# Performance work log

Measured on AMD Instinct MI355X. Metric: run time of the kernel, lower is better.

## Reference

```python
import jax, jax.numpy as jnp
import numpy as np

B, S, N, D, H = 4, 2048, 2048, 1024, 16
HD = D // H  # 64
EPS = 1e-5


def layer_norm(x, w, b):
    m = x.mean(axis=-1, keepdims=True)
    v = ((x - m) ** 2).mean(axis=-1, keepdims=True)
    return (x - m) / jnp.sqrt(v + EPS) * w + b


def setup_inputs() -> dict:
    key = jax.random.key(0)
    ks = jax.random.split(key, 4)
    x_q = jax.random.normal(ks[0], (B, S, D), dtype=jnp.float32)
    x_k = jax.random.normal(ks[1], (B, N, HD), dtype=jnp.float32)
    x_v = jax.random.normal(ks[2], (B, N, HD), dtype=jnp.float32)
    # learned params
    qn_w = jnp.ones((HD,), jnp.float32)
    qn_b = jnp.zeros((HD,), jnp.float32)
    kn_w = jnp.ones((HD,), jnp.float32)
    kn_b = jnp.zeros((HD,), jnp.float32)
    n_w = jnp.ones((D,), jnp.float32)
    n_b = jnp.zeros((D,), jnp.float32)
    # xavier-uniform proj weight (D, D), no bias (proj_bias=False)
    limit = np.sqrt(6.0 / (D + D))
    proj_w = jax.random.uniform(ks[3], (D, D), jnp.float32, -limit, limit)
    return {"x_q": x_q, "x_k": x_k, "x_v": x_v,
            "qn_w": qn_w, "qn_b": qn_b, "kn_w": kn_w, "kn_b": kn_b,
            "n_w": n_w, "n_b": n_b, "proj_w": proj_w}


def reference(x_q, x_k, x_v, qn_w, qn_b, kn_w, kn_b, n_w, n_b, proj_w):
    scale = HD ** -0.5
    # faithful to torch: q.reshape(B, H, -1, head_dim) -- NO transpose before reshape
    q = x_q.reshape(B, H, S, HD)
    q = layer_norm(q, qn_w, qn_b)
    k = layer_norm(x_k, kn_w, kn_b)
    q = q * scale
    attn = jnp.einsum('bhsd,bnd->bhsn', q, k)  # (B,H,S,N) shared K across heads
    attn = jax.nn.softmax(attn, axis=-1)
    x = jnp.einsum('bhsn,bnd->bhsd', attn, x_v)  # shared V across heads
    x = jnp.transpose(x, (0, 2, 1, 3)).reshape(B, S, D)
    x = layer_norm(x, n_w, n_b)
    x = x @ proj_w.T  # nn.Linear: x W^T
    return x
```

## Files before the change

### kernel.cpp

```cpp
#include <hip/hip_runtime.h>

#define B_ 4
#define S_ 2048
#define N_ 2048
#define H_ 16
#define D_ 1024

typedef short s4v __attribute__((ext_vector_type(4)));
typedef short s8v __attribute__((ext_vector_type(8)));
typedef float f4v __attribute__((ext_vector_type(4)));

__device__ __forceinline__ float bf2f(short s) {
  unsigned u = ((unsigned)(unsigned short)s) << 16;
  float f; __builtin_memcpy(&f, &u, 4); return f;
}
__device__ __forceinline__ short f2bf(float f) {
  unsigned u; __builtin_memcpy(&u, &f, 4);
  u += 0x7fffu + ((u >> 16) & 1u);
  return (short)(u >> 16);
}
__device__ __forceinline__ unsigned pack2bf(float a, float b) {
  unsigned ua, ub;
  __builtin_memcpy(&ua, &a, 4);
  __builtin_memcpy(&ub, &b, 4);
  return __builtin_amdgcn_perm(ub + 0x8000u, ua + 0x8000u, 0x07060302u);
}
__device__ __forceinline__ unsigned pk2(float a, float b) {
  unsigned ua, ub;
  __builtin_memcpy(&ua, &a, 4);
  __builtin_memcpy(&ub, &b, 4);
  return __builtin_amdgcn_perm(ub, ua, 0x07060302u);
}
__device__ __forceinline__ s8v load8f32(const float* p) {
  const f4v* q = (const f4v*)p;
  f4v a = q[0], b = q[1];
  union { s8v v; unsigned u[4]; } o;
  o.u[0] = pack2bf(a[0], a[1]); o.u[1] = pack2bf(a[2], a[3]);
  o.u[2] = pack2bf(b[0], b[1]); o.u[3] = pack2bf(b[2], b[3]);
  return o.v;
}

__global__ __launch_bounds__(256) void prep_kernel(
    const float* __restrict__ xk, const float* __restrict__ knw,
    const float* __restrict__ knb, short* __restrict__ kws,
    const float* __restrict__ xv, short* __restrict__ vtp) {
  __shared__ __align__(16) short vstage[4][2048];
  int blk = blockIdx.x;
  if (blk < 2048) {
    int gid = blk * 256 + threadIdx.x;
    int row = gid >> 6, lane = gid & 63;
    float v = xk[(size_t)row * 64 + lane];
    float s = v;
    #pragma unroll
    for (int mm = 1; mm < 64; mm <<= 1) s += __shfl_xor(s, mm, 64);
    float mean = s * 0.015625f;
    float d = v - mean;
    float vs = d * d;
    #pragma unroll
    for (int mm = 1; mm < 64; mm <<= 1) vs += __shfl_xor(vs, mm, 64);
    float rstd = rsqrtf(vs * 0.015625f + 1e-5f);
    kws[(size_t)row * 72 + lane] = f2bf(d * rstd * knw[lane] + knb[lane]);
  } else {
    int wave = threadIdx.x >> 6, lane = threadIdx.x & 63;
    int u = (blk - 2048) * 4 + wave;
    int b = u >> 6, nb = u & 63;
    int r = lane >> 1, dh = lane & 1;
    const float* src = xv + ((size_t)(b * N_ + nb * 32 + r)) * 64 + dh * 32;
    int qq = (r & 15) >> 2;
    int slot = ((r >> 4) << 2) + (r & 3);
    short* wbase = &vstage[wave][0];
    #pragma unroll
    for (int jj = 0; jj < 32; jj += 4) {
      f4v f = *(const f4v*)(src + jj);
      #pragma unroll
      for (int e = 0; e < 4; e++) {
        int d = dh * 32 + jj + e;
        wbase[d * 32 + qq * 8 + slot] = f2bf(f[e]);
      }
    }
    __syncthreads();
    s8v* dst = (s8v*)(vtp + (size_t)u * 2048 + lane * 32);
    const s8v* sp = (const s8v*)(wbase + lane * 32);
    dst[0] = sp[0]; dst[1] = sp[1]; dst[2] = sp[2]; dst[3] = sp[3];
  }
}

__global__ __launch_bounds__(256, 4) void flash_kernel(
    const float* __restrict__ xq, const float* __restrict__ qnw,
    const float* __restrict__ qnb, const short* __restrict__ kws,
    const short* __restrict__ vtp, short* __restrict__ aout) {
  __shared__ union {
    char qs[128 * 144];
    struct { char k[9216]; char v[8192]; } kv;
  } lds;
  int blk = blockIdx.x;
  int sblk = blk & 15, bh = blk >> 4, b = bh >> 4;
  int t = threadIdx.x, wave = t >> 6, lane = t & 63;
  int m = lane & 15, q = lane >> 4;
  const float QSCALE = 0.125f * 1.4426950408889634f;

  {
    int r = t >> 1, half = t & 1;
    const float* qr = xq + ((size_t)bh * S_ + sblk * 128 + r) * 64 + half * 32;
    f4v f[8];
    float s = 0.f, ss = 0.f;
    #pragma unroll
    for (int i = 0; i < 8; i++) {
      f[i] = *(const f4v*)(qr + i * 4);
      s += (f[i][0] + f[i][1]) + (f[i][2] + f[i][3]);
      ss += (f[i][0] * f[i][0] + f[i][1] * f[i][1]) + (f[i][2] * f[i][2] + f[i][3] * f[i][3]);
    }
    s += __shfl_xor(s, 1, 64);
    ss += __shfl_xor(ss, 1, 64);
    float mean = s * 0.015625f;
    float rstd = rsqrtf(ss * 0.015625f - mean * mean + 1e-5f);
    #pragma unroll
    for (int i = 0; i < 4; i++) {
      float y[8];
      #pragma unroll
      for (int e = 0; e < 4; e++) {
        int gi = half * 32 + i * 8;
        y[e]     = ((f[2 * i][e]     - mean) * rstd * qnw[gi + e]     + qnb[gi + e])     * QSCALE;
        y[4 + e] = ((f[2 * i + 1][e] - mean) * rstd * qnw[gi + 4 + e] + qnb[gi + 4 + e]) * QSCALE;
      }
      union { s8v v; unsigned u[4]; } o8;
      #pragma unroll
      for (int e = 0; e < 4; e++) o8.u[e] = pack2bf(y[2 * e], y[2 * e + 1]);
      *(s8v*)(lds.qs + r * 144 + half * 64 + i * 16) = o8.v;
    }
  }
  __syncthreads();

  s8v qlo[2], qhi[2];
  #pragma unroll
  for (int mt = 0; mt < 2; mt++) {
    const char* qrow = lds.qs + (wave * 32 + mt * 16 + m) * 144;
    qlo[mt] = *(const s8v*)(qrow + q * 16);
    qhi[mt] = *(const s8v*)(qrow + 64 + q * 16);
  }

  f4v zero4 = {0.f, 0.f, 0.f, 0.f};
  f4v o[2][4], lacc[2];
  #pragma unroll
  for (int mt = 0; mt < 2; mt++) {
    lacc[mt] = zero4;
    #pragma unroll
    for (int tt = 0; tt < 4; tt++) o[mt][tt] = zero4;
  }
  s8v ones;
  #pragma unroll
  for (int e = 0; e < 8; e++) ones[e] = (short)0x3F80;

  const char* kb = (const char*)kws + (size_t)b * N_ * 144;
  const char* vb = (const char*)vtp + (size_t)b * 64 * 4096;

  for (int c0 = 0; c0 < N_; c0 += 64) {
    const char* kg = kb + (size_t)c0 * 144;
    const char* vg = vb + (size_t)(c0 >> 5) * 4096;
    s8v k0 = *(const s8v*)(kg + t * 16);
    s8v k1 = *(const s8v*)(kg + 4096 + t * 16);
    s8v k2 = {};
    if (t < 64) k2 = *(const s8v*)(kg + 8192 + t * 16);
    s8v v0 = *(const s8v*)(vg + t * 16);
    s8v v1 = *(const s8v*)(vg + 4096 + t * 16);
    __syncthreads();
    *(s8v*)(lds.kv.k + t * 16) = k0;
    *(s8v*)(lds.kv.k + 4096 + t * 16) = k1;
    if (t < 64) *(s8v*)(lds.kv.k + 8192 + t * 16) = k2;
    *(s8v*)(lds.kv.v + t * 16) = v0;
    *(s8v*)(lds.kv.v + 4096 + t * 16) = v1;
    __syncthreads();

    #pragma unroll
    for (int g = 0; g < 2; g++) {
      s8v a0lo = *(const s8v*)(lds.kv.k + (g * 32 + m) * 144 + q * 16);
      s8v a0hi = *(const s8v*)(lds.kv.k + (g * 32 + m) * 144 + 64 + q * 16);
      s8v a1lo = *(const s8v*)(lds.kv.k + (g * 32 + 16 + m) * 144 + q * 16);
      s8v a1hi = *(const s8v*)(lds.kv.k + (g * 32 + 16 + m) * 144 + 64 + q * 16);
      s8v vf[4];
      #pragma unroll
      for (int tt = 0; tt < 4; tt++)
        vf[tt] = *(const s8v*)(lds.kv.v + g * 4096 + (tt * 16 + m) * 64 + q * 16);

      #pragma unroll
      for (int mt = 0; mt < 2; mt++) {
        f4v s0 = zero4, s1 = zero4;
        s0 = __builtin_amdgcn_mfma_f32_16x16x32_bf16(a0lo, qlo[mt], s0, 0, 0, 0);
        s0 = __builtin_amdgcn_mfma_f32_16x16x32_bf16(a0hi, qhi[mt], s0, 0, 0, 0);
        s1 = __builtin_amdgcn_mfma_f32_16x16x32_bf16(a1lo, qlo[mt], s1, 0, 0, 0);
        s1 = __builtin_amdgcn_mfma_f32_16x16x32_bf16(a1hi, qhi[mt], s1, 0, 0, 0);
        float p[8];
        #pragma unroll
        for (int i = 0; i < 4; i++) {
          p[i]     = __builtin_amdgcn_exp2f(fminf(s0[i], 64.0f));
          p[4 + i] = __builtin_amdgcn_exp2f(fminf(s1[i], 64.0f));
        }
        union { s8v v; unsigned u[4]; } pa;
        #pragma unroll
        for (int i = 0; i < 4; i++) pa.u[i] = pk2(p[2 * i], p[2 * i + 1]);
        lacc[mt] = __builtin_amdgcn_mfma_f32_16x16x32_bf16(pa.v, ones, lacc[mt], 0, 0, 0);
        #pragma unroll
        for (int tt = 0; tt < 4; tt++)
          o[mt][tt] = __builtin_amdgcn_mfma_f32_16x16x32_bf16(pa.v, vf[tt], o[mt][tt], 0, 0, 0);
      }
    }
  }

  #pragma unroll
  for (int mt = 0; mt < 2; mt++) {
    #pragma unroll
    for (int i = 0; i < 4; i++) {
      float inv = __builtin_amdgcn_rcpf(lacc[mt][i]);
      int srow = sblk * 128 + wave * 32 + mt * 16 + q * 4 + i;
      size_t orow = ((size_t)b * S_ + srow) * D_ + (size_t)(bh & 15) * 64;
      #pragma unroll
      for (int tt = 0; tt < 4; tt++)
        aout[orow + tt * 16 + m] = f2bf(o[mt][tt][i] * inv);
    }
  }
}

__global__ __launch_bounds__(256) void ln_d_kernel(
    const short* __restrict__ x, const float* __restrict__ w,
    const float* __restrict__ bb, short* __restrict__ y) {
  __shared__ float red[8];
  int row = blockIdx.x, t = threadIdx.x;
  int wave = t >> 6, lane = t & 63;
  const short* xr = x + (size_t)row * D_;
  s4v xv = *(const s4v*)(xr + t * 4);
  float f0 = bf2f(xv[0]), f1 = bf2f(xv[1]), f2 = bf2f(xv[2]), f3 = bf2f(xv[3]);
  float s = (f0 + f1) + (f2 + f3);
  float ss = (f0 * f0 + f1 * f1) + (f2 * f2 + f3 * f3);
  #pragma unroll
  for (int mm = 1; mm < 64; mm <<= 1) {
    s += __shfl_xor(s, mm, 64);
    ss += __shfl_xor(ss, mm, 64);
  }
  if (lane == 0) { red[wave] = s; red[4 + wave] = ss; }
  __syncthreads();
  s = (red[0] + red[1]) + (red[2] + red[3]);
  ss = (red[4] + red[5]) + (red[6] + red[7]);
  float mean = s * (1.0f / 1024.0f);
  float rstd = rsqrtf(ss * (1.0f / 1024.0f) - mean * mean + 1e-5f);
  float fs[4] = {f0, f1, f2, f3};
  s4v yv;
  #pragma unroll
  for (int e = 0; e < 4; e++)
    yv[e] = f2bf((fs[e] - mean) * rstd * w[t * 4 + e] + bb[t * 4 + e]);
  *(s4v*)(y + (size_t)row * D_ + t * 4) = yv;
}

__global__ __launch_bounds__(256) void proj_gemm(
    const short* __restrict__ A, const float* __restrict__ Bw,
    float* __restrict__ C) {
  __shared__ __align__(16) char la[128 * 80];
  __shared__ __align__(16) char lb[128 * 80];
  int bm = (blockIdx.x >> 3) * 128;
  int bn = (blockIdx.x & 7) * 128;
  int wave = threadIdx.x >> 6, lane = threadIdx.x & 63;
  int m = lane & 15, q = lane >> 4;
  int wm = (wave & 1) * 64, wn = (wave >> 1) * 64;
  f4v zero4 = {0.f, 0.f, 0.f, 0.f};
  f4v acc[4][4];
  #pragma unroll
  for (int i = 0; i < 4; i++)
    #pragma unroll
    for (int j = 0; j < 4; j++) acc[i][j] = zero4;
  int sr = threadIdx.x >> 1, sh = (threadIdx.x & 1) * 16;
  for (int k0 = 0; k0 < 1024; k0 += 32) {
    s8v a0 = *(const s8v*)(A + (size_t)(bm + sr) * 1024 + k0 + sh);
    s8v a1 = *(const s8v*)(A + (size_t)(bm + sr) * 1024 + k0 + sh + 8);
    s8v b0 = load8f32(Bw + (size_t)(bn + sr) * 1024 + k0 + sh);
    s8v b1 = load8f32(Bw + (size_t)(bn + sr) * 1024 + k0 + sh + 8);
    __syncthreads();
    *(s8v*)(la + sr * 80 + sh * 2) = a0;
    *(s8v*)(la + sr * 80 + sh * 2 + 16) = a1;
    *(s8v*)(lb + sr * 80 + sh * 2) = b0;
    *(s8v*)(lb + sr * 80 + sh * 2 + 16) = b1;
    __syncthreads();
    s8v af[4], bfv[4];
    #pragma unroll
    for (int i = 0; i < 4; i++) af[i] = *(const s8v*)(la + (wm + i * 16 + m) * 80 + q * 16);
    #pragma unroll
    for (int j = 0; j < 4; j++) bfv[j] = *(const s8v*)(lb + (wn + j * 16 + m) * 80 + q * 16);
    #pragma unroll
    for (int i = 0; i < 4; i++)
      #pragma unroll
      for (int j = 0; j < 4; j++)
        acc[i][j] = __builtin_amdgcn_mfma_f32_16x16x32_bf16(af[i], bfv[j], acc[i][j], 0, 0, 0);
  }
  #pragma unroll
  for (int i = 0; i < 4; i++)
    #pragma unroll
    for (int j = 0; j < 4; j++)
      #pragma unroll
      for (int r = 0; r < 4; r++) {
        int row = bm + wm + i * 16 + q * 4 + r;
        int col = bn + wn + j * 16 + m;
        C[(size_t)row * 1024 + col] = acc[i][j][r];
      }
}

extern "C" void kernel_launch(void* const* d_in, const int* in_sizes, int n_in,
                              void* d_out, int out_size, void* d_ws, size_t ws_size,
                              hipStream_t stream) {
  const float* xq  = (const float*)d_in[0];
  const float* xk  = (const float*)d_in[1];
  const float* xv  = (const float*)d_in[2];
  const float* qnw = (const float*)d_in[3];
  const float* qnb = (const float*)d_in[4];
  const float* knw = (const float*)d_in[5];
  const float* knb = (const float*)d_in[6];
  const float* nw  = (const float*)d_in[7];
  const float* nb  = (const float*)d_in[8];
  const float* pw  = (const float*)d_in[9];
  float* out = (float*)d_out;

  short* kws = (short*)d_ws;
  short* vtp = (short*)((char*)d_ws + 0x120000);
  short* yws = (short*)d_ws;
  short* aout = (short*)d_out;

  prep_kernel<<<2112, 256, 0, stream>>>(xk, knw, knb, kws, xv, vtp);
  flash_kernel<<<1024, 256, 0, stream>>>(xq, qnw, qnb, kws, vtp, aout);
  ln_d_kernel<<<B_ * S_, 256, 0, stream>>>(aout, nw, nb, yws);
  proj_gemm<<<512, 256, 0, stream>>>(yws, pw, out);
}
```

Before: 233.2 us.

## Double-buffer K/V tiles in LDS with async global-to-LDS loads

The flash kernel's K/V staging now uses global_load_lds to copy tiles straight from global memory into LDS, with two buffers. The next chunk is prefetched while the current one is consumed, and the first V tile is issued before the Q layernorm. This removes the register round-trip and one of the two barriers per iteration, so load latency can overlap with the MFMA and exp work. In exchange the kernel uses roughly twice the LDS, which may limit occupancy. Correctness relies on the compiler inserting the right vmcnt waits before the barrier for the async LDS writes.

After: 236.7 us. Within noise of the previous version (+1.5%).

```diff
diff --git a/kernel.cpp b/kernel.cpp
--- a/kernel.cpp
+++ b/kernel.cpp
@@ -38,6 +38,11 @@
   o.u[0] = pack2bf(a[0], a[1]); o.u[1] = pack2bf(a[2], a[3]);
   o.u[2] = pack2bf(b[0], b[1]); o.u[3] = pack2bf(b[2], b[3]);
   return o.v;
+}
+__device__ __forceinline__ void gld16(const char* g, char* l) {
+  __builtin_amdgcn_global_load_lds(
+      (const __attribute__((address_space(1))) unsigned*)g,
+      (__attribute__((address_space(3))) unsigned*)l, 16, 0, 0);
 }
 
 __global__ __launch_bounds__(256) void prep_kernel(
@@ -89,9 +94,9 @@
     const float* __restrict__ xq, const float* __restrict__ qnw,
     const float* __restrict__ qnb, const short* __restrict__ kws,
     const short* __restrict__ vtp, short* __restrict__ aout) {
-  __shared__ union {
+  __shared__ __align__(16) union {
     char qs[128 * 144];
-    struct { char k[9216]; char v[8192]; } kv;
+    struct { char k[2][9216]; char v[2][8192]; } kv;
   } lds;
   int blk = blockIdx.x;
   int sblk = blk & 15, bh = blk >> 4, b = bh >> 4;
@@ -99,6 +104,12 @@
   int m = lane & 15, q = lane >> 4;
   const float QSCALE = 0.125f * 1.4426950408889634f;
 
+  const char* kb = (const char*)kws + (size_t)b * N_ * 144;
+  const char* vb = (const char*)vtp + (size_t)b * 64 * 4096;
+
+  gld16(vb + t * 16,        lds.kv.v[0] + t * 16);
+  gld16(vb + 4096 + t * 16, lds.kv.v[0] + 4096 + t * 16);
+
   {
     int r = t >> 1, half = t & 1;
     const float* qr = xq + ((size_t)bh * S_ + sblk * 128 + r) * 64 + half * 32;
@@ -138,6 +149,12 @@
     qlo[mt] = *(const s8v*)(qrow + q * 16);
     qhi[mt] = *(const s8v*)(qrow + 64 + q * 16);
   }
+  __syncthreads();
+
+  gld16(kb + t * 16,        lds.kv.k[0] + t * 16);
+  gld16(kb + 4096 + t * 16, lds.kv.k[0] + 4096 + t * 16);
+  if (t < 64) gld16(kb + 8192 + t * 16, lds.kv.k[0] + 8192 + t * 16);
+  __syncthreads();
 
   f4v zero4 = {0.f, 0.f, 0.f, 0.f};
   f4v o[2][4], lacc[2];
@@ -151,36 +168,32 @@
   #pragma unroll
   for (int e = 0; e < 8; e++) ones[e] = (short)0x3F80;
 
-  const char* kb = (const char*)kws + (size_t)b * N_ * 144;
-  const char* vb = (const char*)vtp + (size_t)b * 64 * 4096;
-
-  for (int c0 = 0; c0 < N_; c0 += 64) {
-    const char* kg = kb + (size_t)c0 * 144;
-    const char* vg = vb + (size_t)(c0 >> 5) * 4096;
-    s8v k0 = *(const s8v*)(kg + t * 16);
-    s8v k1 = *(const s8v*)(kg + 4096 + t * 16);
-    s8v k2 = {};
-    if (t < 64) k2 = *(const s8v*)(kg + 8192 + t * 16);
-    s8v v0 = *(const s8v*)(vg + t * 16);
-    s8v v1 = *(const s8v*)(vg + 4096 + t * 16);
-    __syncthreads();
-    *(s8v*)(lds.kv.k + t * 16) = k0;
-    *(s8v*)(lds.kv.k + 4096 + t * 16) = k1;
-    if (t < 64) *(s8v*)(lds.kv.k + 8192 + t * 16) = k2;
-    *(s8v*)(lds.kv.v + t * 16) = v0;
-    *(s8v*)(lds.kv.v + 4096 + t * 16) = v1;
-    __syncthreads();
+  for (int it = 0; it < 32; ++it) {
+    int cur = it & 1;
+    if (it < 31) {
+      const char* kg = kb + (size_t)(it + 1) * 9216;
+      const char* vg = vb + (size_t)(it + 1) * 8192;
+      char* kd = lds.kv.k[cur ^ 1];
+      char* vd = lds.kv.v[cur ^ 1];
+      gld16(kg + t * 16,        kd + t * 16);
+      gld16(kg + 4096 + t * 16, kd + 4096 + t * 16);
+      if (t < 64) gld16(kg + 8192 + t * 16, kd + 8192 + t * 16);
+      gld16(vg + t * 16,        vd + t * 16);
+      gld16(vg + 4096 + t * 16, vd + 4096 + t * 16);
+    }
+    const char* kc = lds.kv.k[cur];
+    const char* vc = lds.kv.v[cur];
 
     #pragma unroll
     for (int g = 0; g < 2; g++) {
-      s8v a0lo = *(const s8v*)(lds.kv.k + (g * 32 + m) * 144 + q * 16);
-      s8v a0hi = *(const s8v*)(lds.kv.k + (g * 32 + m) * 144 + 64 + q * 16);
-      s8v a1lo = *(const s8v*)(lds.kv.k + (g * 32 + 16 + m) * 144 + q * 16);
-      s8v a1hi = *(const s8v*)(lds.kv.k + (g * 32 + 16 + m) * 144 + 64 + q * 16);
+      s8v a0lo = *(const s8v*)(kc + (g * 32 + m) * 144 + q * 16);
+      s8v a0hi = *(const s8v*)(kc + (g * 32 + m) * 144 + 64 + q * 16);
+      s8v a1lo = *(const s8v*)(kc + (g * 32 + 16 + m) * 144 + q * 16);
+      s8v a1hi = *(const s8v*)(kc + (g * 32 + 16 + m) * 144 + 64 + q * 16);
       s8v vf[4];
       #pragma unroll
       for (int tt = 0; tt < 4; tt++)
-        vf[tt] = *(const s8v*)(lds.kv.v + g * 4096 + (tt * 16 + m) * 64 + q * 16);
+        vf[tt] = *(const s8v*)(vc + g * 4096 + (tt * 16 + m) * 64 + q * 16);
 
       #pragma unroll
       for (int mt = 0; mt < 2; mt++) {
@@ -204,6 +217,7 @@
           o[mt][tt] = __builtin_amdgcn_mfma_f32_16x16x32_bf16(pa.v, vf[tt], o[mt][tt], 0, 0, 0);
       }
     }
+    __syncthreads();
   }
 
   #pragma unroll
```
